# Kernel tuning notes

Measured on AMD Instinct MI355X. Metric: run time of the kernel, lower is better.

The kernel has to match this reference:

```python
import jax, jax.numpy as jnp
import numpy as np

DIM = 1024
HEADS = 16
HEAD_DIM = DIM // HEADS
EPS = 1e-6


def setup_inputs() -> dict:
    key = jax.random.key(0)
    ks = jax.random.split(key, 4)
    x = jax.random.normal(ks[0], (2, 2048, DIM), dtype=jnp.float32)
    W_qkv = jax.random.normal(ks[1], (3 * DIM, DIM), dtype=jnp.float32) * (DIM ** -0.5)
    q_gamma = jnp.ones((HEAD_DIM,), jnp.float32)
    q_beta = jnp.zeros((HEAD_DIM,), jnp.float32)
    k_gamma = jnp.ones((HEAD_DIM,), jnp.float32)
    k_beta = jnp.zeros((HEAD_DIM,), jnp.float32)
    W_proj = jax.random.normal(ks[2], (DIM, DIM), dtype=jnp.float32) * (DIM ** -0.5)
    b_proj = jnp.zeros((DIM,), jnp.float32)
    return {"x": x, "W_qkv": W_qkv, "q_gamma": q_gamma, "q_beta": q_beta,
            "k_gamma": k_gamma, "k_beta": k_beta, "W_proj": W_proj, "b_proj": b_proj}


def _layernorm(x, gamma, beta):
    mu = jnp.mean(x, axis=-1, keepdims=True)
    var = jnp.mean(jnp.square(x - mu), axis=-1, keepdims=True)
    return (x - mu) * jax.lax.rsqrt(var + EPS) * gamma + beta


def reference(x, W_qkv, q_gamma, q_beta, k_gamma, k_beta, W_proj, b_proj):
    B, N, C = x.shape
    H, D = HEADS, HEAD_DIM
    scale = D ** -0.5
    qkv = jnp.einsum('bnc,oc->bno', x, W_qkv)            # [B,N,3C]
    qkv = qkv.reshape(B, N, 3, H, D).transpose(2, 0, 3, 1, 4)  # [3,B,H,N,D]
    q, k, v = qkv[0], qkv[1], qkv[2]
    q = _layernorm(q, q_gamma, q_beta)
    k = _layernorm(k, k_gamma, k_beta)
    attn = jnp.einsum('bhnd,bhmd->bhnm', q * scale, k)   # [B,H,N,N]
    attn = jax.nn.softmax(attn, axis=-1)
    out = jnp.einsum('bhnm,bhmd->bhnd', attn, v)         # [B,H,N,D]
    out = out.transpose(0, 2, 1, 3).reshape(B, N, C)
    return jnp.einsum('bnc,oc->bno', out, W_proj) + b_proj
```

## Files before the change

### kernel.cpp

```cpp
#include <hip/hip_runtime.h>

#define DIM 1024
#define HEADS 16
#define HD 64
#define BATCH 2
#define SEQ 2048
#define ROWS (BATCH*SEQ)
#define EPS 1e-6f

typedef float f32x4  __attribute__((ext_vector_type(4)));
typedef float f32x16 __attribute__((ext_vector_type(16)));
typedef short s16x4  __attribute__((ext_vector_type(4)));
typedef short s16x8  __attribute__((ext_vector_type(8)));

static __device__ __forceinline__ short f2bf(float f) {
    union { float f; unsigned u; } x; x.f = f;
    unsigned r = x.u + 0x7FFFu + ((x.u >> 16) & 1u);
    return (short)(r >> 16);
}
static __device__ __forceinline__ s16x8 pack8(float4 lo, float4 hi) {
    s16x8 r;
    r[0]=f2bf(lo.x); r[1]=f2bf(lo.y); r[2]=f2bf(lo.z); r[3]=f2bf(lo.w);
    r[4]=f2bf(hi.x); r[5]=f2bf(hi.y); r[6]=f2bf(hi.z); r[7]=f2bf(hi.w);
    return r;
}
static __device__ __forceinline__ unsigned cvtpk(float a, float b) {
    unsigned r;
    asm("v_cvt_pk_bf16_f32 %0, %1, %2" : "=v"(r) : "v"(a), "v"(b));
    return r;
}
static __device__ __forceinline__ void gld16(short* l, const short* g) {
    __builtin_amdgcn_global_load_lds(
        (const __attribute__((address_space(1))) void*)g,
        (__attribute__((address_space(3))) void*)l, 16, 0, 0);
}

#define MFMA32(A,B,C) __builtin_amdgcn_mfma_f32_32x32x16_bf16(A, B, C, 0, 0, 0)
#define MFMA16(A,B,C) __builtin_amdgcn_mfma_f32_16x16x32_bf16(A, B, C, 0, 0, 0)

__global__ __launch_bounds__(256) void convert3(
    const float* __restrict__ x, const float* __restrict__ wq,
    const float* __restrict__ wp,
    short* __restrict__ xb, short* __restrict__ wqb, short* __restrict__ wpb)
{
    const int idx = blockIdx.x * 256 + threadIdx.x;
    const int C1 = 4194304/8, C2 = 3145728/8;
    const float* src; short* dst; int off;
    if (idx < C1)            { src = x;  dst = xb;  off = idx; }
    else if (idx < C1 + C2)  { src = wq; dst = wqb; off = idx - C1; }
    else                     { src = wp; dst = wpb; off = idx - C1 - C2; }
    float4 a = ((const float4*)src)[off*2];
    float4 b = ((const float4*)src)[off*2 + 1];
    ((s16x8*)dst)[off] = pack8(a, b);
}

#define BKG 64

template<int MODE>
__global__ __launch_bounds__(256) void gemm_bf16(
    const short* __restrict__ A, const short* __restrict__ W,
    const float* __restrict__ bias,
    const float* __restrict__ qg, const float* __restrict__ qbeta,
    const float* __restrict__ kg, const float* __restrict__ kbeta,
    short* __restrict__ qb, short* __restrict__ kb, short* __restrict__ vb,
    float* __restrict__ out)
{
    alignas(16) __shared__ short As[128*BKG];
    alignas(16) __shared__ short Bs[128*BKG];
    const int tid  = threadIdx.x;
    const int lane = tid & 63, wave = tid >> 6;
    const int wr = wave >> 1, wc = wave & 1;
    const int c = lane & 15, g = lane >> 4;
    const int brow = blockIdx.y * 128, bcol = blockIdx.x * 128;

    const int srow = lane >> 3;
    const int scol = (lane & 7) * 8;
    const short* ag = A + (size_t)(brow + srow)*DIM + scol;
    const short* wg = W + (size_t)(bcol + srow)*DIM + scol;

    f32x4 acc[4][4] = {};

    for (int k0 = 0; k0 < DIM; k0 += BKG) {
        #pragma unroll
        for (int j = 0; j < 4; j++) {
            const int rg = (wave*4 + j) * 8;
            gld16(&As[rg*BKG], ag + (size_t)rg*DIM + k0);
            gld16(&Bs[rg*BKG], wg + (size_t)rg*DIM + k0);
        }
        __syncthreads();

        #pragma unroll
        for (int ks = 0; ks < 2; ks++) {
            s16x8 af[4], bf[4];
            #pragma unroll
            for (int m = 0; m < 4; m++)
                af[m] = *(const s16x8*)&As[(wr*64 + m*16 + c)*BKG + ks*32 + g*8];
            #pragma unroll
            for (int n = 0; n < 4; n++)
                bf[n] = *(const s16x8*)&Bs[(wc*64 + n*16 + c)*BKG + ks*32 + g*8];
            #pragma unroll
            for (int m = 0; m < 4; m++)
                #pragma unroll
                for (int n = 0; n < 4; n++)
                    acc[m][n] = MFMA16(af[m], bf[n], acc[m][n]);
        }
        __syncthreads();
    }

    if (MODE == 0) {
        const int colbase = bcol + wc*64;
        const int t = colbase >> 10;
        const int h = (colbase >> 6) & 15;
        short* dst = (t == 0) ? qb : (t == 1) ? kb : vb;
        float gam[4], bet[4];
        float scale = 1.0f;
        if (t < 2) {
            const float* G  = (t == 0) ? qg : kg;
            const float* Bt = (t == 0) ? qbeta : kbeta;
            #pragma unroll
            for (int n = 0; n < 4; n++) { gam[n] = G[n*16 + c]; bet[n] = Bt[n*16 + c]; }
            if (t == 0) scale = 0.125f * 1.44269504088896340736f;
        }
        #pragma unroll
        for (int m = 0; m < 4; m++) {
            #pragma unroll
            for (int j = 0; j < 4; j++) {
                const int row = brow + wr*64 + m*16 + g*4 + j;
                const int bi = row >> 11, ni = row & (SEQ-1);
                const size_t rb = ((size_t)(bi*HEADS + h)*SEQ + ni)*HD;
                float v0 = acc[m][0][j], v1 = acc[m][1][j];
                float v2 = acc[m][2][j], v3 = acc[m][3][j];
                if (t < 2) {
                    float s = (v0 + v1) + (v2 + v3);
                    s += __shfl_xor(s, 1); s += __shfl_xor(s, 2);
                    s += __shfl_xor(s, 4); s += __shfl_xor(s, 8);
                    const float mu = s * 0.015625f;
                    v0 -= mu; v1 -= mu; v2 -= mu; v3 -= mu;
                    float vv = (v0*v0 + v1*v1) + (v2*v2 + v3*v3);
                    vv += __shfl_xor(vv, 1); vv += __shfl_xor(vv, 2);
                    vv += __shfl_xor(vv, 4); vv += __shfl_xor(vv, 8);
                    const float rstd = rsqrtf(vv * 0.015625f + EPS);
                    v0 = (v0*rstd*gam[0] + bet[0]) * scale;
                    v1 = (v1*rstd*gam[1] + bet[1]) * scale;
                    v2 = (v2*rstd*gam[2] + bet[2]) * scale;
                    v3 = (v3*rstd*gam[3] + bet[3]) * scale;
                }
                dst[rb + 0*16 + c] = f2bf(v0);
                dst[rb + 1*16 + c] = f2bf(v1);
                dst[rb + 2*16 + c] = f2bf(v2);
                dst[rb + 3*16 + c] = f2bf(v3);
            }
        }
    } else {
        #pragma unroll
        for (int n = 0; n < 4; n++) {
            const int col = bcol + wc*64 + n*16 + c;
            const float bv = bias[col];
            #pragma unroll
            for (int m = 0; m < 4; m++) {
                #pragma unroll
                for (int j = 0; j < 4; j++) {
                    const int row = brow + wr*64 + m*16 + g*4 + j;
                    out[(size_t)row*DIM + col] = acc[m][n][j] + bv;
                }
            }
        }
    }
}

__global__ __launch_bounds__(256) void repack_kv(
    const short* __restrict__ kin, const short* __restrict__ vin,
    short* __restrict__ KP, short* __restrict__ VP)
{
    constexpr int LT = 72;
    alignas(16) __shared__ short Kl[64*LT];
    alignas(16) __shared__ short Vl[64*LT];
    const int bh = blockIdx.x, n0 = blockIdx.y * 64;
    const int tid = threadIdx.x;
    const int r = tid >> 2, cq = (tid & 3) * 16;
    {
        const short* ksrc = kin + ((size_t)bh*SEQ + n0 + r)*HD + cq;
        const short* vsrc = vin + ((size_t)bh*SEQ + n0 + r)*HD + cq;
        *(s16x8*)&Kl[r*LT + cq]     = *(const s16x8*)ksrc;
        *(s16x8*)&Kl[r*LT + cq + 8] = *(const s16x8*)(ksrc + 8);
        *(s16x8*)&Vl[r*LT + cq]     = *(const s16x8*)vsrc;
        *(s16x8*)&Vl[r*LT + cq + 8] = *(const s16x8*)(vsrc + 8);
    }
    __syncthreads();
    const int tt = tid >> 7;
    const int r2 = tid & 127;
    const int sub = r2 >> 5, lp = r2 & 31;
    const size_t tbase = ((size_t)bh*64 + blockIdx.y*2 + tt)*2048 + sub*512;
    #pragma unroll
    for (int g2 = 0; g2 < 2; g2++) {
        const int lane = 2*lp + g2;
        s16x8 val = *(const s16x8*)&Kl[(tt*32 + (lane & 31))*LT + sub*16 + 8*(lane >> 5)];
        *(s16x8*)&KP[tbase + lane*8] = val;
    }
    #pragma unroll
    for (int g2 = 0; g2 < 2; g2++) {
        const int lane = 2*lp + g2;
        const int hi = lane >> 5, l31 = lane & 31;
        s16x8 val;
        #pragma unroll
        for (int e = 0; e < 8; e++)
            val[e] = Vl[(tt*32 + (sub >> 1)*16 + 8*hi + e)*LT + (sub & 1)*32 + l31];
        *(s16x8*)&VP[tbase + lane*8] = val;
    }
}

__global__ __launch_bounds__(256) void attn_kernel(
    const short* __restrict__ qbuf, const short* __restrict__ KP,
    const short* __restrict__ VP, short* __restrict__ aout)
{
    alignas(16) __shared__ float OL[2][64][32];
    __shared__ float ML[2][2][64];

    const int bh = blockIdx.x, qt = blockIdx.y;
    const int tid = threadIdx.x, wave = tid >> 6, lane = tid & 63;
    const int qsub = wave >> 1, half = wave & 1;
    const int l31 = lane & 31, hi = lane >> 5;
    const int q0 = qt*64 + qsub*32;

    s16x8 qf[4];
    const short* qrow = qbuf + ((size_t)bh*SEQ + q0 + l31)*HD + 8*hi;
    #pragma unroll
    for (int ks = 0; ks < 4; ks++) qf[ks] = *(const s16x8*)(qrow + 16*ks);

    const short* kp = KP + ((size_t)bh*64 + half*32)*2048 + lane*8;
    const short* vp = VP + ((size_t)bh*64 + half*32)*2048 + lane*8;

    s16x8 kc0 = *(const s16x8*)(kp);
    s16x8 kc1 = *(const s16x8*)(kp + 512);
    s16x8 kc2 = *(const s16x8*)(kp + 1024);
    s16x8 kc3 = *(const s16x8*)(kp + 1536);
    s16x8 vc0 = *(const s16x8*)(vp);
    s16x8 vc1 = *(const s16x8*)(vp + 512);
    s16x8 vc2 = *(const s16x8*)(vp + 1024);
    s16x8 vc3 = *(const s16x8*)(vp + 1536);

    f32x16 o0 = {}, o1 = {};
    float m = -1e30f, l = 0.f;

    for (int it = 0; it < 32; it++) {
        f32x16 s = {};
        __builtin_amdgcn_s_setprio(1);
        s = MFMA32(kc0, qf[0], s);
        s = MFMA32(kc1, qf[1], s);
        s = MFMA32(kc2, qf[2], s);
        s = MFMA32(kc3, qf[3], s);
        __builtin_amdgcn_s_setprio(0);

        const int nt = ((it + 1) & 31) * 2048;
        kc0 = *(const s16x8*)(kp + nt);
        kc1 = *(const s16x8*)(kp + nt + 512);
        kc2 = *(const s16x8*)(kp + nt + 1024);
        kc3 = *(const s16x8*)(kp + nt + 1536);
        __builtin_amdgcn_sched_barrier(0);

        float t8[8];
        #pragma unroll
        for (int i = 0; i < 8; i++) t8[i] = fmaxf(s[i], s[i+8]);
        #pragma unroll
        for (int i = 0; i < 4; i++) t8[i] = fmaxf(t8[i], t8[i+4]);
        float pmax = fmaxf(fmaxf(t8[0], t8[2]), fmaxf(t8[1], t8[3]));
        pmax = fmaxf(pmax, __shfl_xor(pmax, 32));

        if (!__all(pmax - m <= 8.0f)) {
            float mn = fmaxf(m, pmax);
            float corr = exp2f(m - mn);
            #pragma unroll
            for (int i = 0; i < 16; i++) { o0[i] *= corr; o1[i] *= corr; }
            l *= corr;
            m = mn;
        }
        #pragma unroll
        for (int i = 0; i < 16; i++) s[i] = exp2f(s[i] - m);
        float a8[8];
        #pragma unroll
        for (int i = 0; i < 8; i++) a8[i] = s[i] + s[i+8];
        #pragma unroll
        for (int i = 0; i < 4; i++) a8[i] += a8[i+4];
        float rs = (a8[0] + a8[2]) + (a8[1] + a8[3]);
        rs += __shfl_xor(rs, 32);
        l += rs;

        s16x8 pa0, pa1;
        {
            unsigned A0 = cvtpk(s[0], s[1]),  A1 = cvtpk(s[2], s[3]);
            unsigned B0 = cvtpk(s[4], s[5]),  B1 = cvtpk(s[6], s[7]);
            asm volatile("v_permlane32_swap_b32 %0, %1" : "+v"(A0), "+v"(B0));
            asm volatile("v_permlane32_swap_b32 %0, %1" : "+v"(A1), "+v"(B1));
            union { s16x8 v; unsigned u[4]; } w;
            w.u[0]=A0; w.u[1]=A1; w.u[2]=B0; w.u[3]=B1;
            pa0 = w.v;
            unsigned C0 = cvtpk(s[8], s[9]),   C1 = cvtpk(s[10], s[11]);
            unsigned D0 = cvtpk(s[12], s[13]), D1 = cvtpk(s[14], s[15]);
            asm volatile("v_permlane32_swap_b32 %0, %1" : "+v"(C0), "+v"(D0));
            asm volatile("v_permlane32_swap_b32 %0, %1" : "+v"(C1), "+v"(D1));
            union { s16x8 v; unsigned u[4]; } w2;
            w2.u[0]=C0; w2.u[1]=C1; w2.u[2]=D0; w2.u[3]=D1;
            pa1 = w2.v;
        }

        __builtin_amdgcn_s_setprio(1);
        o0 = MFMA32(vc0, pa0, o0);
        o1 = MFMA32(vc1, pa0, o1);
        o0 = MFMA32(vc2, pa1, o0);
        o1 = MFMA32(vc3, pa1, o1);
        __builtin_amdgcn_s_setprio(0);

        vc0 = *(const s16x8*)(vp + nt);
        vc1 = *(const s16x8*)(vp + nt + 512);
        vc2 = *(const s16x8*)(vp + nt + 1024);
        vc3 = *(const s16x8*)(vp + nt + 1536);
    }

    if (half == 1) {
        float* ob = &OL[qsub][lane][0];
        #pragma unroll
        for (int i = 0; i < 8; i++) {
            const int slot = (i + (lane & 7)) & 7;
            f32x4 v;
            if (i < 4) { v[0]=o0[4*i]; v[1]=o0[4*i+1]; v[2]=o0[4*i+2]; v[3]=o0[4*i+3]; }
            else { const int j = i-4; v[0]=o1[4*j]; v[1]=o1[4*j+1]; v[2]=o1[4*j+2]; v[3]=o1[4*j+3]; }
            *(f32x4*)(ob + slot*4) = v;
        }
        ML[qsub][0][lane] = m;
        ML[qsub][1][lane] = l;
    }
    __syncthreads();
    if (half == 0) {
        const float m1 = ML[qsub][0][lane];
        const float l1 = ML[qsub][1][lane];
        const float ms = fmaxf(m, m1);
        const float c0 = exp2f(m - ms), c1 = exp2f(m1 - ms);
        const float inv = 1.0f / (l*c0 + l1*c1);
        const float* ob = &OL[qsub][lane][0];
        const int b = bh >> 4, h = bh & 15;
        short* dst = aout + ((size_t)(b*SEQ + q0 + l31))*DIM + h*HD;
        #pragma unroll
        for (int i = 0; i < 8; i++) {
            const int slot = (i + (lane & 7)) & 7;
            f32x4 p = *(const f32x4*)(ob + slot*4);
            s16x4 st;
            if (i < 4) {
                #pragma unroll
                for (int j = 0; j < 4; j++) st[j] = f2bf((o0[4*i+j]*c0 + p[j]*c1) * inv);
                *(s16x4*)(dst + 8*i + 4*hi) = st;
            } else {
                const int t3 = i - 4;
                #pragma unroll
                for (int j = 0; j < 4; j++) st[j] = f2bf((o1[4*t3+j]*c0 + p[j]*c1) * inv);
                *(s16x4*)(dst + 32 + 8*t3 + 4*hi) = st;
            }
        }
    }
}

extern "C" void kernel_launch(void* const* d_in, const int* in_sizes, int n_in,
                              void* d_out, int out_size, void* d_ws, size_t ws_size,
                              hipStream_t stream)
{
    const float* x     = (const float*)d_in[0];
    const float* Wqkv  = (const float*)d_in[1];
    const float* qg    = (const float*)d_in[2];
    const float* qbeta = (const float*)d_in[3];
    const float* kg    = (const float*)d_in[4];
    const float* kbeta = (const float*)d_in[5];
    const float* Wproj = (const float*)d_in[6];
    const float* bproj = (const float*)d_in[7];
    float* out = (float*)d_out;

    char* ws = (char*)d_ws;
    const size_t MB = 1024*1024;
    short* xb     = (short*)(ws);
    short* KP     = (short*)(ws);
    short* wqkvb  = (short*)(ws + 8*MB);
    short* wprojb = (short*)(ws + 14*MB);
    short* q      = (short*)(ws + 16*MB);
    short* k      = (short*)(ws + 24*MB);
    short* aout   = (short*)(ws + 24*MB);
    short* vrow   = (short*)(ws + 32*MB);
    short* VP     = (short*)(ws + 40*MB);

    convert3<<<dim3(4096), 256, 0, stream>>>(x, Wqkv, Wproj, xb, wqkvb, wprojb);

    gemm_bf16<0><<<dim3(3*DIM/128, ROWS/128), 256, 0, stream>>>(
        xb, wqkvb, nullptr, qg, qbeta, kg, kbeta, q, k, vrow, nullptr);

    repack_kv<<<dim3(BATCH*HEADS, SEQ/64), 256, 0, stream>>>(k, vrow, KP, VP);

    attn_kernel<<<dim3(BATCH*HEADS, SEQ/64), 256, 0, stream>>>(q, KP, VP, aout);

    gemm_bf16<1><<<dim3(DIM/128, ROWS/128), 256, 0, stream>>>(
        aout, wprojb, bproj, nullptr, nullptr, nullptr, nullptr,
        nullptr, nullptr, nullptr, out);
}
```

Measured before the change: 147.6 us.

## Process two 32-row query tiles per wave in attention to reuse K/V fragments

Each attention wave now handles 64 query rows, as two 32-row sub-tiles A and B, instead of 32. Every K and V fragment loaded from global memory therefore feeds twice as many MFMAs. The grid is halved along the sequence axis, and the LDS merge buffers grow to hold both sub-tiles. This cuts K/V load traffic per unit of compute and interleaves independent MFMA chains. In exchange it raises register pressure (four accumulators) and halves the block count, to 512 blocks, which may reduce occupancy.

```diff
diff --git a/kernel.cpp b/kernel.cpp
--- a/kernel.cpp
+++ b/kernel.cpp
@@ -37,6 +37,42 @@
 
 #define MFMA32(A,B,C) __builtin_amdgcn_mfma_f32_32x32x16_bf16(A, B, C, 0, 0, 0)
 #define MFMA16(A,B,C) __builtin_amdgcn_mfma_f32_16x16x32_bf16(A, B, C, 0, 0, 0)
+
+struct PA { s16x8 a, b; };
+static __device__ __forceinline__ PA packP(const f32x16& s) {
+    PA r;
+    unsigned A0 = cvtpk(s[0], s[1]),  A1 = cvtpk(s[2], s[3]);
+    unsigned B0 = cvtpk(s[4], s[5]),  B1 = cvtpk(s[6], s[7]);
+    asm volatile("v_permlane32_swap_b32 %0, %1" : "+v"(A0), "+v"(B0));
+    asm volatile("v_permlane32_swap_b32 %0, %1" : "+v"(A1), "+v"(B1));
+    union { s16x8 v; unsigned u[4]; } w;
+    w.u[0]=A0; w.u[1]=A1; w.u[2]=B0; w.u[3]=B1;
+    r.a = w.v;
+    unsigned C0 = cvtpk(s[8], s[9]),   C1 = cvtpk(s[10], s[11]);
+    unsigned D0 = cvtpk(s[12], s[13]), D1 = cvtpk(s[14], s[15]);
+    asm volatile("v_permlane32_swap_b32 %0, %1" : "+v"(C0), "+v"(D0));
+    asm volatile("v_permlane32_swap_b32 %0, %1" : "+v"(C1), "+v"(D1));
+    union { s16x8 v; unsigned u[4]; } w2;
+    w2.u[0]=C0; w2.u[1]=C1; w2.u[2]=D0; w2.u[3]=D1;
+    r.b = w2.v;
+    return r;
+}
+static __device__ __forceinline__ float tree_max(const f32x16& s) {
+    float t[8];
+    #pragma unroll
+    for (int i = 0; i < 8; i++) t[i] = fmaxf(s[i], s[i+8]);
+    #pragma unroll
+    for (int i = 0; i < 4; i++) t[i] = fmaxf(t[i], t[i+4]);
+    return fmaxf(fmaxf(t[0], t[2]), fmaxf(t[1], t[3]));
+}
+static __device__ __forceinline__ float tree_sum(const f32x16& s) {
+    float t[8];
+    #pragma unroll
+    for (int i = 0; i < 8; i++) t[i] = s[i] + s[i+8];
+    #pragma unroll
+    for (int i = 0; i < 4; i++) t[i] += t[i+4];
+    return (t[0] + t[2]) + (t[1] + t[3]);
+}
 
 __global__ __launch_bounds__(256) void convert3(
     const float* __restrict__ x, const float* __restrict__ wq,
@@ -213,19 +249,24 @@
     const short* __restrict__ qbuf, const short* __restrict__ KP,
     const short* __restrict__ VP, short* __restrict__ aout)
 {
-    alignas(16) __shared__ float OL[2][64][32];
-    __shared__ float ML[2][2][64];
-
-    const int bh = blockIdx.x, qt = blockIdx.y;
+    alignas(16) __shared__ float OL[2][64][64];
+    __shared__ float ML[2][4][64];
+
+    const int bh = blockIdx.x, qgrp = blockIdx.y;
     const int tid = threadIdx.x, wave = tid >> 6, lane = tid & 63;
-    const int qsub = wave >> 1, half = wave & 1;
+    const int qg = wave >> 1, half = wave & 1;
     const int l31 = lane & 31, hi = lane >> 5;
-    const int q0 = qt*64 + qsub*32;
-
-    s16x8 qf[4];
-    const short* qrow = qbuf + ((size_t)bh*SEQ + q0 + l31)*HD + 8*hi;
-    #pragma unroll
-    for (int ks = 0; ks < 4; ks++) qf[ks] = *(const s16x8*)(qrow + 16*ks);
+    const int q0 = qgrp*128 + qg*64;
+
+    s16x8 qfA[4], qfB[4];
+    {
+        const short* qrowA = qbuf + ((size_t)bh*SEQ + q0 + l31)*HD + 8*hi;
+        #pragma unroll
+        for (int ks = 0; ks < 4; ks++) {
+            qfA[ks] = *(const s16x8*)(qrowA + 16*ks);
+            qfB[ks] = *(const s16x8*)(qrowA + 32*HD + 16*ks);
+        }
+    }
 
     const short* kp = KP + ((size_t)bh*64 + half*32)*2048 + lane*8;
     const short* vp = VP + ((size_t)bh*64 + half*32)*2048 + lane*8;
@@ -239,16 +280,16 @@
     s16x8 vc2 = *(const s16x8*)(vp + 1024);
     s16x8 vc3 = *(const s16x8*)(vp + 1536);
 
-    f32x16 o0 = {}, o1 = {};
-    float m = -1e30f, l = 0.f;
+    f32x16 oA0 = {}, oA1 = {}, oB0 = {}, oB1 = {};
+    float mA = -1e30f, mB = -1e30f, lA = 0.f, lB = 0.f;
 
     for (int it = 0; it < 32; it++) {
-        f32x16 s = {};
+        f32x16 sA = {}, sB = {};
         __builtin_amdgcn_s_setprio(1);
-        s = MFMA32(kc0, qf[0], s);
-        s = MFMA32(kc1, qf[1], s);
-        s = MFMA32(kc2, qf[2], s);
-        s = MFMA32(kc3, qf[3], s);
+        sA = MFMA32(kc0, qfA[0], sA);  sB = MFMA32(kc0, qfB[0], sB);
+        sA = MFMA32(kc1, qfA[1], sA);  sB = MFMA32(kc1, qfB[1], sB);
+        sA = MFMA32(kc2, qfA[2], sA);  sB = MFMA32(kc2, qfB[2], sB);
+        sA = MFMA32(kc3, qfA[3], sA);  sB = MFMA32(kc3, qfB[3], sB);
         __builtin_amdgcn_s_setprio(0);
 
         const int nt = ((it + 1) & 31) * 2048;
@@ -258,56 +299,42 @@
         kc3 = *(const s16x8*)(kp + nt + 1536);
         __builtin_amdgcn_sched_barrier(0);
 
-        float t8[8];
-        #pragma unroll
-        for (int i = 0; i < 8; i++) t8[i] = fmaxf(s[i], s[i+8]);
-        #pragma unroll
-        for (int i = 0; i < 4; i++) t8[i] = fmaxf(t8[i], t8[i+4]);
-        float pmax = fmaxf(fmaxf(t8[0], t8[2]), fmaxf(t8[1], t8[3]));
-        pmax = fmaxf(pmax, __shfl_xor(pmax, 32));
-
-        if (!__all(pmax - m <= 8.0f)) {
-            float mn = fmaxf(m, pmax);
-            float corr = exp2f(m - mn);
-            #pragma unroll
-            for (int i = 0; i < 16; i++) { o0[i] *= corr; o1[i] *= corr; }
-            l *= corr;
-            m = mn;
-        }
-        #pragma unroll
-        for (int i = 0; i < 16; i++) s[i] = exp2f(s[i] - m);
-        float a8[8];
-        #pragma unroll
-        for (int i = 0; i < 8; i++) a8[i] = s[i] + s[i+8];
-        #pragma unroll
-        for (int i = 0; i < 4; i++) a8[i] += a8[i+4];
-        float rs = (a8[0] + a8[2]) + (a8[1] + a8[3]);
-        rs += __shfl_xor(rs, 32);
-        l += rs;
-
-        s16x8 pa0, pa1;
-        {
-            unsigned A0 = cvtpk(s[0], s[1]),  A1 = cvtpk(s[2], s[3]);
-            unsigned B0 = cvtpk(s[4], s[5]),  B1 = cvtpk(s[6], s[7]);
-            asm volatile("v_permlane32_swap_b32 %0, %1" : "+v"(A0), "+v"(B0));
-            asm volatile("v_permlane32_swap_b32 %0, %1" : "+v"(A1), "+v"(B1));
-            union { s16x8 v; unsigned u[4]; } w;
-            w.u[0]=A0; w.u[1]=A1; w.u[2]=B0; w.u[3]=B1;
-            pa0 = w.v;
-            unsigned C0 = cvtpk(s[8], s[9]),   C1 = cvtpk(s[10], s[11]);
-            unsigned D0 = cvtpk(s[12], s[13]), D1 = cvtpk(s[14], s[15]);
-            asm volatile("v_permlane32_swap_b32 %0, %1" : "+v"(C0), "+v"(D0));
-            asm volatile("v_permlane32_swap_b32 %0, %1" : "+v"(C1), "+v"(D1));
-            union { s16x8 v; unsigned u[4]; } w2;
-            w2.u[0]=C0; w2.u[1]=C1; w2.u[2]=D0; w2.u[3]=D1;
-            pa1 = w2.v;
-        }
+        float pmaxA = tree_max(sA);
+        pmaxA = fmaxf(pmaxA, __shfl_xor(pmaxA, 32));
+        float pmaxB = tree_max(sB);
+        pmaxB = fmaxf(pmaxB, __shfl_xor(pmaxB, 32));
+
+        if (!__all((pmaxA - mA <= 8.0f) && (pmaxB - mB <= 8.0f))) {
+            float mnA = fmaxf(mA, pmaxA), mnB = fmaxf(mB, pmaxB);
+            float cA = exp2f(mA - mnA), cB = exp2f(mB - mnB);
+            #pragma unroll
+            for (int i = 0; i < 16; i++) {
+                oA0[i] *= cA; oA1[i] *= cA;
+                oB0[i] *= cB; oB1[i] *= cB;
+            }
+            lA *= cA; lB *= cB;
+            mA = mnA; mB = mnB;
+        }
+        #pragma unroll
+        for (int i = 0; i < 16; i++) {
+            sA[i] = exp2f(sA[i] - mA);
+            sB[i] = exp2f(sB[i] - mB);
+        }
+        float rsA = tree_sum(sA);
+        rsA += __shfl_xor(rsA, 32);
+        lA += rsA;
+        float rsB = tree_sum(sB);
+        rsB += __shfl_xor(rsB, 32);
+        lB += rsB;
+
+        PA paA = packP(sA);
+        PA paB = packP(sB);
 
         __builtin_amdgcn_s_setprio(1);
-        o0 = MFMA32(vc0, pa0, o0);
-        o1 = MFMA32(vc1, pa0, o1);
-        o0 = MFMA32(vc2, pa1, o0);
-        o1 = MFMA32(vc3, pa1, o1);
+        oA0 = MFMA32(vc0, paA.a, oA0);  oB0 = MFMA32(vc0, paB.a, oB0);
+        oA1 = MFMA32(vc1, paA.a, oA1);  oB1 = MFMA32(vc1, paB.a, oB1);
+        oA0 = MFMA32(vc2, paA.b, oA0);  oB0 = MFMA32(vc2, paB.b, oB0);
+        oA1 = MFMA32(vc3, paA.b, oA1);  oB1 = MFMA32(vc3, paB.b, oB1);
         __builtin_amdgcn_s_setprio(0);
 
         vc0 = *(const s16x8*)(vp + nt);
@@ -317,42 +344,58 @@
     }
 
     if (half == 1) {
-        float* ob = &OL[qsub][lane][0];
-        #pragma unroll
-        for (int i = 0; i < 8; i++) {
-            const int slot = (i + (lane & 7)) & 7;
+        float* ob = &OL[qg][lane][0];
+        #pragma unroll
+        for (int i = 0; i < 16; i++) {
+            const int slot = (i + (lane & 15)) & 15;
             f32x4 v;
-            if (i < 4) { v[0]=o0[4*i]; v[1]=o0[4*i+1]; v[2]=o0[4*i+2]; v[3]=o0[4*i+3]; }
-            else { const int j = i-4; v[0]=o1[4*j]; v[1]=o1[4*j+1]; v[2]=o1[4*j+2]; v[3]=o1[4*j+3]; }
+            if (i < 4)       { const int t=i;    v[0]=oA0[4*t]; v[1]=oA0[4*t+1]; v[2]=oA0[4*t+2]; v[3]=oA0[4*t+3]; }
+            else if (i < 8)  { const int t=i-4;  v[0]=oA1[4*t]; v[1]=oA1[4*t+1]; v[2]=oA1[4*t+2]; v[3]=oA1[4*t+3]; }
+            else if (i < 12) { const int t=i-8;  v[0]=oB0[4*t]; v[1]=oB0[4*t+1]; v[2]=oB0[4*t+2]; v[3]=oB0[4*t+3]; }
+            else             { const int t=i-12; v[0]=oB1[4*t]; v[1]=oB1[4*t+1]; v[2]=oB1[4*t+2]; v[3]=oB1[4*t+3]; }
             *(f32x4*)(ob + slot*4) = v;
         }
-        ML[qsub][0][lane] = m;
-        ML[qsub][1][lane] = l;
+        ML[qg][0][lane] = mA; ML[qg][1][lane] = lA;
+        ML[qg][2][lane] = mB; ML[qg][3][lane] = lB;
     }
     __syncthreads();
     if (half == 0) {
-        const float m1 = ML[qsub][0][lane];
-        const float l1 = ML[qsub][1][lane];
-        const float ms = fmaxf(m, m1);
-        const float c0 = exp2f(m - ms), c1 = exp2f(m1 - ms);
-        const float inv = 1.0f / (l*c0 + l1*c1);
-        const float* ob = &OL[qsub][lane][0];
+        const float mA1 = ML[qg][0][lane], lA1 = ML[qg][1][lane];
+        const float mB1 = ML[qg][2][lane], lB1 = ML[qg][3][lane];
+        const float msA = fmaxf(mA, mA1), msB = fmaxf(mB, mB1);
+        const float cA0 = exp2f(mA - msA), cA1 = exp2f(mA1 - msA);
+        const float cB0 = exp2f(mB - msB), cB1 = exp2f(mB1 - msB);
+        const float invA = 1.0f / (lA*cA0 + lA1*cA1);
+        const float invB = 1.0f / (lB*cB0 + lB1*cB1);
         const int b = bh >> 4, h = bh & 15;
-        short* dst = aout + ((size_t)(b*SEQ + q0 + l31))*DIM + h*HD;
-        #pragma unroll
-        for (int i = 0; i < 8; i++) {
-            const int slot = (i + (lane & 7)) & 7;
+        short* dstA = aout + ((size_t)(b*SEQ + q0 + l31))*DIM + h*HD;
+        short* dstB = dstA + (size_t)32*DIM;
+        const float* ob = &OL[qg][lane][0];
+        #pragma unroll
+        for (int i = 0; i < 16; i++) {
+            const int slot = (i + (lane & 15)) & 15;
             f32x4 p = *(const f32x4*)(ob + slot*4);
             s16x4 st;
             if (i < 4) {
-                #pragma unroll
-                for (int j = 0; j < 4; j++) st[j] = f2bf((o0[4*i+j]*c0 + p[j]*c1) * inv);
-                *(s16x4*)(dst + 8*i + 4*hi) = st;
+                const int t = i;
+                #pragma unroll
+                for (int j = 0; j < 4; j++) st[j] = f2bf((oA0[4*t+j]*cA0 + p[j]*cA1) * invA);
+                *(s16x4*)(dstA + 8*t + 4*hi) = st;
+            } else if (i < 8) {
+                const int t = i - 4;
+                #pragma unroll
+                for (int j = 0; j < 4; j++) st[j] = f2bf((oA1[4*t+j]*cA0 + p[j]*cA1) * invA);
+                *(s16x4*)(dstA + 32 + 8*t + 4*hi) = st;
+            } else if (i < 12) {
+                const int t = i - 8;
+                #pragma unroll
+                for (int j = 0; j < 4; j++) st[j] = f2bf((oB0[4*t+j]*cB0 + p[j]*cB1) * invB);
+                *(s16x4*)(dstB + 8*t + 4*hi) = st;
             } else {
-                const int t3 = i - 4;
-                #pragma unroll
-                for (int j = 0; j < 4; j++) st[j] = f2bf((o1[4*t3+j]*c0 + p[j]*c1) * inv);
-                *(s16x4*)(dst + 32 + 8*t3 + 4*hi) = st;
+                const int t = i - 12;
+                #pragma unroll
+                for (int j = 0; j < 4; j++) st[j] = f2bf((oB1[4*t+j]*cB0 + p[j]*cB1) * invB);
+                *(s16x4*)(dstB + 32 + 8*t + 4*hi) = st;
             }
         }
     }
@@ -391,7 +434,7 @@
 
     repack_kv<<<dim3(BATCH*HEADS, SEQ/64), 256, 0, stream>>>(k, vrow, KP, VP);
 
-    attn_kernel<<<dim3(BATCH*HEADS, SEQ/64), 256, 0, stream>>>(q, KP, VP, aout);
+    attn_kernel<<<dim3(BATCH*HEADS, SEQ/128), 256, 0, stream>>>(q, KP, VP, aout);
 
     gemm_bf16<1><<<dim3(DIM/128, ROWS/128), 256, 0, stream>>>(
         aout, wprojb, bproj, nullptr, nullptr, nullptr, nullptr,
```

New measurement: 166.2 us. 12.6% more time.

## Fuse K/V repacking into QKV GEMM epilogue and drop repack kernel

Applied to the files above, without the earlier changes.

The QKV GEMM epilogue now writes K and V straight into the tiled, MFMA-ready layouts the attention kernel consumes, so the separate repack_kv kernel and its extra global round trip are removed. The workspace is remapped so aout reuses the xb region. The attention kernel also gets a launch-bounds occupancy hint of 4, and its inline max/sum/pack code is moved into helper functions. The trade-off is that the epilogue now issues scattered 2-byte stores with strided addresses, especially for V, which may write less efficiently than the old row stores.

```diff
diff --git a/kernel.cpp b/kernel.cpp
--- a/kernel.cpp
+++ b/kernel.cpp
@@ -37,6 +37,42 @@
 
 #define MFMA32(A,B,C) __builtin_amdgcn_mfma_f32_32x32x16_bf16(A, B, C, 0, 0, 0)
 #define MFMA16(A,B,C) __builtin_amdgcn_mfma_f32_16x16x32_bf16(A, B, C, 0, 0, 0)
+
+struct PA { s16x8 a, b; };
+static __device__ __forceinline__ PA packP(const f32x16& s) {
+    PA r;
+    unsigned A0 = cvtpk(s[0], s[1]),  A1 = cvtpk(s[2], s[3]);
+    unsigned B0 = cvtpk(s[4], s[5]),  B1 = cvtpk(s[6], s[7]);
+    asm volatile("v_permlane32_swap_b32 %0, %1" : "+v"(A0), "+v"(B0));
+    asm volatile("v_permlane32_swap_b32 %0, %1" : "+v"(A1), "+v"(B1));
+    union { s16x8 v; unsigned u[4]; } w;
+    w.u[0]=A0; w.u[1]=A1; w.u[2]=B0; w.u[3]=B1;
+    r.a = w.v;
+    unsigned C0 = cvtpk(s[8], s[9]),   C1 = cvtpk(s[10], s[11]);
+    unsigned D0 = cvtpk(s[12], s[13]), D1 = cvtpk(s[14], s[15]);
+    asm volatile("v_permlane32_swap_b32 %0, %1" : "+v"(C0), "+v"(D0));
+    asm volatile("v_permlane32_swap_b32 %0, %1" : "+v"(C1), "+v"(D1));
+    union { s16x8 v; unsigned u[4]; } w2;
+    w2.u[0]=C0; w2.u[1]=C1; w2.u[2]=D0; w2.u[3]=D1;
+    r.b = w2.v;
+    return r;
+}
+static __device__ __forceinline__ float tree_max(const f32x16& s) {
+    float t[8];
+    #pragma unroll
+    for (int i = 0; i < 8; i++) t[i] = fmaxf(s[i], s[i+8]);
+    #pragma unroll
+    for (int i = 0; i < 4; i++) t[i] = fmaxf(t[i], t[i+4]);
+    return fmaxf(fmaxf(t[0], t[2]), fmaxf(t[1], t[3]));
+}
+static __device__ __forceinline__ float tree_sum(const f32x16& s) {
+    float t[8];
+    #pragma unroll
+    for (int i = 0; i < 8; i++) t[i] = s[i] + s[i+8];
+    #pragma unroll
+    for (int i = 0; i < 4; i++) t[i] += t[i+4];
+    return (t[0] + t[2]) + (t[1] + t[3]);
+}
 
 __global__ __launch_bounds__(256) void convert3(
     const float* __restrict__ x, const float* __restrict__ wq,
@@ -62,7 +98,7 @@
     const float* __restrict__ bias,
     const float* __restrict__ qg, const float* __restrict__ qbeta,
     const float* __restrict__ kg, const float* __restrict__ kbeta,
-    short* __restrict__ qb, short* __restrict__ kb, short* __restrict__ vb,
+    short* __restrict__ qb, short* __restrict__ kpb, short* __restrict__ vpb,
     float* __restrict__ out)
 {
     alignas(16) __shared__ short As[128*BKG];
@@ -111,7 +147,6 @@
         const int colbase = bcol + wc*64;
         const int t = colbase >> 10;
         const int h = (colbase >> 6) & 15;
-        short* dst = (t == 0) ? qb : (t == 1) ? kb : vb;
         float gam[4], bet[4];
         float scale = 1.0f;
         if (t < 2) {
@@ -127,7 +162,7 @@
             for (int j = 0; j < 4; j++) {
                 const int row = brow + wr*64 + m*16 + g*4 + j;
                 const int bi = row >> 11, ni = row & (SEQ-1);
-                const size_t rb = ((size_t)(bi*HEADS + h)*SEQ + ni)*HD;
+                const int bh = bi*HEADS + h;
                 float v0 = acc[m][0][j], v1 = acc[m][1][j];
                 float v2 = acc[m][2][j], v3 = acc[m][3][j];
                 if (t < 2) {
@@ -145,10 +180,30 @@
                     v2 = (v2*rstd*gam[2] + bet[2]) * scale;
                     v3 = (v3*rstd*gam[3] + bet[3]) * scale;
                 }
-                dst[rb + 0*16 + c] = f2bf(v0);
-                dst[rb + 1*16 + c] = f2bf(v1);
-                dst[rb + 2*16 + c] = f2bf(v2);
-                dst[rb + 3*16 + c] = f2bf(v3);
+                if (t == 0) {
+                    const size_t rb = ((size_t)bh*SEQ + ni)*HD;
+                    qb[rb + 0*16 + c] = f2bf(v0);
+                    qb[rb + 1*16 + c] = f2bf(v1);
+                    qb[rb + 2*16 + c] = f2bf(v2);
+                    qb[rb + 3*16 + c] = f2bf(v3);
+                } else {
+                    const size_t tb = ((size_t)bh*64 + (ni >> 5)) * 2048;
+                    const int kl = ni & 31;
+                    if (t == 1) {
+                        const size_t b2 = tb + (size_t)(((c >> 3)*32 + kl)*8 + (c & 7));
+                        kpb[b2 + 0*512] = f2bf(v0);
+                        kpb[b2 + 1*512] = f2bf(v1);
+                        kpb[b2 + 2*512] = f2bf(v2);
+                        kpb[b2 + 3*512] = f2bf(v3);
+                    } else {
+                        const int hi2 = (kl & 15) >> 3, e2 = kl & 7;
+                        const size_t b0 = tb + (size_t)((2*(kl >> 4))*512 + (hi2*32)*8 + e2);
+                        vpb[b0 + (size_t)(c)*8]        = f2bf(v0);
+                        vpb[b0 + (size_t)(16 + c)*8]   = f2bf(v1);
+                        vpb[b0 + 512 + (size_t)(c)*8]      = f2bf(v2);
+                        vpb[b0 + 512 + (size_t)(16 + c)*8] = f2bf(v3);
+                    }
+                }
             }
         }
     } else {
@@ -168,48 +223,7 @@
     }
 }
 
-__global__ __launch_bounds__(256) void repack_kv(
-    const short* __restrict__ kin, const short* __restrict__ vin,
-    short* __restrict__ KP, short* __restrict__ VP)
-{
-    constexpr int LT = 72;
-    alignas(16) __shared__ short Kl[64*LT];
-    alignas(16) __shared__ short Vl[64*LT];
-    const int bh = blockIdx.x, n0 = blockIdx.y * 64;
-    const int tid = threadIdx.x;
-    const int r = tid >> 2, cq = (tid & 3) * 16;
-    {
-        const short* ksrc = kin + ((size_t)bh*SEQ + n0 + r)*HD + cq;
-        const short* vsrc = vin + ((size_t)bh*SEQ + n0 + r)*HD + cq;
-        *(s16x8*)&Kl[r*LT + cq]     = *(const s16x8*)ksrc;
-        *(s16x8*)&Kl[r*LT + cq + 8] = *(const s16x8*)(ksrc + 8);
-        *(s16x8*)&Vl[r*LT + cq]     = *(const s16x8*)vsrc;
-        *(s16x8*)&Vl[r*LT + cq + 8] = *(const s16x8*)(vsrc + 8);
-    }
-    __syncthreads();
-    const int tt = tid >> 7;
-    const int r2 = tid & 127;
-    const int sub = r2 >> 5, lp = r2 & 31;
-    const size_t tbase = ((size_t)bh*64 + blockIdx.y*2 + tt)*2048 + sub*512;
-    #pragma unroll
-    for (int g2 = 0; g2 < 2; g2++) {
-        const int lane = 2*lp + g2;
-        s16x8 val = *(const s16x8*)&Kl[(tt*32 + (lane & 31))*LT + sub*16 + 8*(lane >> 5)];
-        *(s16x8*)&KP[tbase + lane*8] = val;
-    }
-    #pragma unroll
-    for (int g2 = 0; g2 < 2; g2++) {
-        const int lane = 2*lp + g2;
-        const int hi = lane >> 5, l31 = lane & 31;
-        s16x8 val;
-        #pragma unroll
-        for (int e = 0; e < 8; e++)
-            val[e] = Vl[(tt*32 + (sub >> 1)*16 + 8*hi + e)*LT + (sub & 1)*32 + l31];
-        *(s16x8*)&VP[tbase + lane*8] = val;
-    }
-}
-
-__global__ __launch_bounds__(256) void attn_kernel(
+__global__ __launch_bounds__(256, 4) void attn_kernel(
     const short* __restrict__ qbuf, const short* __restrict__ KP,
     const short* __restrict__ VP, short* __restrict__ aout)
 {
@@ -258,12 +272,7 @@
         kc3 = *(const s16x8*)(kp + nt + 1536);
         __builtin_amdgcn_sched_barrier(0);
 
-        float t8[8];
-        #pragma unroll
-        for (int i = 0; i < 8; i++) t8[i] = fmaxf(s[i], s[i+8]);
-        #pragma unroll
-        for (int i = 0; i < 4; i++) t8[i] = fmaxf(t8[i], t8[i+4]);
-        float pmax = fmaxf(fmaxf(t8[0], t8[2]), fmaxf(t8[1], t8[3]));
+        float pmax = tree_max(s);
         pmax = fmaxf(pmax, __shfl_xor(pmax, 32));
 
         if (!__all(pmax - m <= 8.0f)) {
@@ -276,38 +285,17 @@
         }
         #pragma unroll
         for (int i = 0; i < 16; i++) s[i] = exp2f(s[i] - m);
-        float a8[8];
-        #pragma unroll
-        for (int i = 0; i < 8; i++) a8[i] = s[i] + s[i+8];
-        #pragma unroll
-        for (int i = 0; i < 4; i++) a8[i] += a8[i+4];
-        float rs = (a8[0] + a8[2]) + (a8[1] + a8[3]);
+        float rs = tree_sum(s);
         rs += __shfl_xor(rs, 32);
         l += rs;
 
-        s16x8 pa0, pa1;
-        {
-            unsigned A0 = cvtpk(s[0], s[1]),  A1 = cvtpk(s[2], s[3]);
-            unsigned B0 = cvtpk(s[4], s[5]),  B1 = cvtpk(s[6], s[7]);
-            asm volatile("v_permlane32_swap_b32 %0, %1" : "+v"(A0), "+v"(B0));
-            asm volatile("v_permlane32_swap_b32 %0, %1" : "+v"(A1), "+v"(B1));
-            union { s16x8 v; unsigned u[4]; } w;
-            w.u[0]=A0; w.u[1]=A1; w.u[2]=B0; w.u[3]=B1;
-            pa0 = w.v;
-            unsigned C0 = cvtpk(s[8], s[9]),   C1 = cvtpk(s[10], s[11]);
-            unsigned D0 = cvtpk(s[12], s[13]), D1 = cvtpk(s[14], s[15]);
-            asm volatile("v_permlane32_swap_b32 %0, %1" : "+v"(C0), "+v"(D0));
-            asm volatile("v_permlane32_swap_b32 %0, %1" : "+v"(C1), "+v"(D1));
-            union { s16x8 v; unsigned u[4]; } w2;
-            w2.u[0]=C0; w2.u[1]=C1; w2.u[2]=D0; w2.u[3]=D1;
-            pa1 = w2.v;
-        }
+        PA pa = packP(s);
 
         __builtin_amdgcn_s_setprio(1);
-        o0 = MFMA32(vc0, pa0, o0);
-        o1 = MFMA32(vc1, pa0, o1);
-        o0 = MFMA32(vc2, pa1, o0);
-        o1 = MFMA32(vc3, pa1, o1);
+        o0 = MFMA32(vc0, pa.a, o0);
+        o1 = MFMA32(vc1, pa.a, o1);
+        o0 = MFMA32(vc2, pa.b, o0);
+        o1 = MFMA32(vc3, pa.b, o1);
         __builtin_amdgcn_s_setprio(0);
 
         vc0 = *(const s16x8*)(vp + nt);
@@ -375,21 +363,17 @@
     char* ws = (char*)d_ws;
     const size_t MB = 1024*1024;
     short* xb     = (short*)(ws);
-    short* KP     = (short*)(ws);
+    short* aout   = (short*)(ws);
     short* wqkvb  = (short*)(ws + 8*MB);
     short* wprojb = (short*)(ws + 14*MB);
     short* q      = (short*)(ws + 16*MB);
-    short* k      = (short*)(ws + 24*MB);
-    short* aout   = (short*)(ws + 24*MB);
-    short* vrow   = (short*)(ws + 32*MB);
-    short* VP     = (short*)(ws + 40*MB);
+    short* KP     = (short*)(ws + 24*MB);
+    short* VP     = (short*)(ws + 32*MB);
 
     convert3<<<dim3(4096), 256, 0, stream>>>(x, Wqkv, Wproj, xb, wqkvb, wprojb);
 
     gemm_bf16<0><<<dim3(3*DIM/128, ROWS/128), 256, 0, stream>>>(
-        xb, wqkvb, nullptr, qg, qbeta, kg, kbeta, q, k, vrow, nullptr);
-
-    repack_kv<<<dim3(BATCH*HEADS, SEQ/64), 256, 0, stream>>>(k, vrow, KP, VP);
+        xb, wqkvb, nullptr, qg, qbeta, kg, kbeta, q, KP, VP, nullptr);
 
     attn_kernel<<<dim3(BATCH*HEADS, SEQ/64), 256, 0, stream>>>(q, KP, VP, aout);
 
```

After: 140.2 us. 1.05x faster.
